# Kernel optimization log

Hardware: AMD Instinct MI355X
Metric: run time of the kernel (lower is better)

## Reference

```python
import jax, jax.numpy as jnp
import numpy as np

B, S, D, H = 2, 2048, 1024, 16
DK = D // H  # 64


def setup_inputs() -> dict:
    key = jax.random.key(0)
    ks = jax.random.split(key, 12)
    inp = {
        "query": jax.random.normal(ks[0], (B, S, D), jnp.float32),
        "key": jax.random.normal(ks[1], (B, S, D), jnp.float32),
        "value": jax.random.normal(ks[2], (B, S, D), jnp.float32),
        "mask": jnp.ones((B, 1, S, S), jnp.float32),  # 1.0 = attend
    }
    sc = 1.0 / np.sqrt(D)
    inp["wq"] = jax.random.normal(ks[3], (D, D), jnp.float32) * sc
    inp["bq"] = jax.random.normal(ks[4], (D,), jnp.float32) * 0.01
    inp["wk"] = jax.random.normal(ks[5], (D, D), jnp.float32) * sc
    inp["bk"] = jax.random.normal(ks[6], (D,), jnp.float32) * 0.01
    inp["wv"] = jax.random.normal(ks[7], (D, D), jnp.float32) * sc
    inp["bv"] = jax.random.normal(ks[8], (D,), jnp.float32) * 0.01
    inp["wo"] = jax.random.normal(ks[9], (D, D), jnp.float32) * sc
    inp["bo"] = jax.random.normal(ks[10], (D,), jnp.float32) * 0.01
    return inp


def _split_heads(x):
    # [B, S, D] -> [B, H, S, DK]
    b, s, _ = x.shape
    return x.reshape(b, s, H, DK).transpose(0, 2, 1, 3)


def reference(query, key, value, mask, wq, bq, wk, bk, wv, bv, wo, bo):
    # Linear projections (torch Linear: x @ W.T + b)
    q = _split_heads(query @ wq.T + bq)   # [B,H,Sq,DK]
    k = _split_heads(key @ wk.T + bk)     # [B,H,Sk,DK]
    v = _split_heads(value @ wv.T + bv)   # [B,H,Sk,DK]

    attn = jnp.einsum('bhqd,bhkd->bhqk', q, k) / jnp.sqrt(jnp.float32(DK))
    # mask: 1.0 attend, 0.0 masked -> add finfo.min at masked positions
    inv = (1.0 - mask) * jnp.finfo(attn.dtype).min
    attn = attn + inv
    attention_weights = jax.nn.softmax(attn, axis=-1)  # [B,H,Sq,Sk]
    # dropout=0.0 (eval mode): identity
    ctx = jnp.einsum('bhqk,bhkd->bhqd', attention_weights, v)  # [B,H,Sq,DK]
    concat = ctx.transpose(0, 2, 1, 3).reshape(ctx.shape[0], ctx.shape[2], D)
    output = concat @ wo.T + bo
    return (output, attention_weights)
```

## Files before the change

### kernel.cpp

```cpp
#include <hip/hip_runtime.h>
#include <cstdint>

typedef short bf16x8 __attribute__((ext_vector_type(8)));
typedef short bf16x4 __attribute__((ext_vector_type(4)));
typedef float f32x4 __attribute__((ext_vector_type(4)));

#define NEG_MAX 3.402823466e38f
#define C_EXP2 0.1803368801111244f

__device__ __forceinline__ unsigned short f2bf(float f) {
  uint32_t u = __builtin_bit_cast(uint32_t, f);
  u += 0x7FFFu + ((u >> 16) & 1u);
  return (unsigned short)(u >> 16);
}

__device__ __forceinline__ float bf2f(unsigned short s) {
  return __builtin_bit_cast(float, (uint32_t)s << 16);
}

__device__ __forceinline__ bf16x8 pack8(float4 x, float4 y) {
  bf16x8 r;
  r[0] = (short)f2bf(x.x); r[1] = (short)f2bf(x.y); r[2] = (short)f2bf(x.z); r[3] = (short)f2bf(x.w);
  r[4] = (short)f2bf(y.x); r[5] = (short)f2bf(y.y); r[6] = (short)f2bf(y.z); r[7] = (short)f2bf(y.w);
  return r;
}

__global__ __launch_bounds__(256) void cvt_w(const float* __restrict__ wq, const float* __restrict__ wk,
                                             const float* __restrict__ wv, const float* __restrict__ wo,
                                             unsigned short* __restrict__ out) {
  int i = blockIdx.x * 256 + threadIdx.x;
  const int sel = i >> 18;
  const int idx = i & 0x3FFFF;
  const float* src = (sel == 0) ? wq : (sel == 1) ? wk : (sel == 2) ? wv : wo;
  float4 v = reinterpret_cast<const float4*>(src)[idx];
  ushort4 o;
  o.x = f2bf(v.x); o.y = f2bf(v.y); o.z = f2bf(v.z); o.w = f2bf(v.w);
  reinterpret_cast<ushort4*>(out)[i] = o;
}

__global__ __launch_bounds__(256) void mask_scan(const float* __restrict__ mask,
                                                 int* __restrict__ flags) {
  const int blk = blockIdx.x;
  const int kt = blk & 31, qt = (blk >> 5) & 31, b = blk >> 10;
  const float* base = mask + ((size_t)b * 2048 + qt * 64) * 2048 + kt * 64;
  const int t = threadIdx.x;
  const int row = t >> 2, c0 = (t & 3) * 16;
  const float4* p = reinterpret_cast<const float4*>(base + (size_t)row * 2048 + c0);
  bool ones = true;
#pragma unroll
  for (int i = 0; i < 4; ++i) {
    float4 v = p[i];
    ones = ones && (v.x == 1.f) && (v.y == 1.f) && (v.z == 1.f) && (v.w == 1.f);
  }
  unsigned long long ball = __ballot(ones);
  __shared__ int sf[4];
  if ((t & 63) == 0) sf[t >> 6] = (ball == ~0ull) ? 1 : 0;
  __syncthreads();
  if (t == 0) flags[blk] = sf[0] & sf[1] & sf[2] & sf[3];
}

__global__ __launch_bounds__(256) void gemm_qkv(const float* __restrict__ Aq,
                                                const float* __restrict__ Ak,
                                                const float* __restrict__ Av,
                                                const unsigned short* __restrict__ W3,
                                                const float* __restrict__ bq,
                                                const float* __restrict__ bk,
                                                const float* __restrict__ bv,
                                                unsigned short* __restrict__ Qbf,
                                                unsigned short* __restrict__ Kbf,
                                                unsigned short* __restrict__ Vtb) {
  constexpr int KD = 1024;
  __shared__ __align__(16) unsigned short Al[128 * 32];
  __shared__ __align__(16) unsigned short Bl[128 * 32];
  const int tid = threadIdx.x;
  const int l = tid & 63;
  const int w = tid >> 6;
  const int lr = l & 15;
  const int lg = l >> 4;
  const int gm = blockIdx.y;
  const int gn = blockIdx.x;
  const int z = blockIdx.z;
  const int wr = w >> 1;
  const int wc = w & 1;

  const float* Af = (z == 0) ? Aq : (z == 1) ? Ak : Av;
  const float* bias = (z == 0) ? bq : (z == 1) ? bk : bv;
  const unsigned short* Bw = W3 + (size_t)z * 1048576;
  unsigned short* Cb = (z == 0) ? Qbf : (z == 1) ? Kbf : Vtb;

  f32x4 acc[4][4];
#pragma unroll
  for (int m = 0; m < 4; ++m)
#pragma unroll
    for (int n = 0; n < 4; ++n) acc[m][n] = (f32x4){0.f, 0.f, 0.f, 0.f};

  const int c0 = w * 2;
  const int srow = (l >> 2);
  const int scol = (l & 3) * 8;
  const unsigned short* gB = Bw + (size_t)(gn * 128) * KD;

  const int arow = tid >> 1;
  const int ahalf = tid & 1;
  const float* gA = Af + (size_t)(gm * 128 + arow) * KD + ahalf * 16;

  float4 ap[4];
  {
    const float4* p = reinterpret_cast<const float4*>(gA);
#pragma unroll
    for (int i = 0; i < 4; ++i) ap[i] = p[i];
  }

  for (int kt = 0; kt < 32; ++kt) {
    const int k0 = kt * 32;
    const unsigned short* b0 = gB + (size_t)(c0 * 16 + srow) * KD + k0 + scol;
    const unsigned short* b1 = b0 + (size_t)16 * KD;
    __builtin_amdgcn_global_load_lds((const __attribute__((address_space(1))) void*)b0,
                                     (__attribute__((address_space(3))) void*)&Bl[c0 * 512], 16, 0, 0);
    __builtin_amdgcn_global_load_lds((const __attribute__((address_space(1))) void*)b1,
                                     (__attribute__((address_space(3))) void*)&Bl[c0 * 512 + 512], 16, 0, 0);
    {
      bf16x8* dst = reinterpret_cast<bf16x8*>(&Al[arow * 32 + ahalf * 16]);
      dst[0] = pack8(ap[0], ap[1]);
      dst[1] = pack8(ap[2], ap[3]);
    }
    __syncthreads();
    if (kt + 1 < 32) {
      const float4* p = reinterpret_cast<const float4*>(gA + (kt + 1) * 32);
#pragma unroll
      for (int i = 0; i < 4; ++i) ap[i] = p[i];
    }
    bf16x8 af[4], bfr[4];
#pragma unroll
    for (int m = 0; m < 4; ++m)
      af[m] = *reinterpret_cast<const bf16x8*>(&Al[(wr * 64 + m * 16 + lr) * 32 + lg * 8]);
#pragma unroll
    for (int n = 0; n < 4; ++n)
      bfr[n] = *reinterpret_cast<const bf16x8*>(&Bl[(wc * 64 + n * 16 + lr) * 32 + lg * 8]);
#pragma unroll
    for (int m = 0; m < 4; ++m)
#pragma unroll
      for (int n = 0; n < 4; ++n)
        acc[m][n] = __builtin_amdgcn_mfma_f32_16x16x32_bf16(af[m], bfr[n], acc[m][n], 0, 0, 0);
    __syncthreads();
  }

#pragma unroll
  for (int m = 0; m < 4; ++m) {
#pragma unroll
    for (int n = 0; n < 4; ++n) {
      const int colg = gn * 128 + wc * 64 + n * 16 + lr;
      const float bv2 = bias[colg];
#pragma unroll
      for (int r = 0; r < 4; ++r) {
        const int rowg = gm * 128 + wr * 64 + m * 16 + lg * 4 + r;
        const float v = acc[m][n][r] + bv2;
        const int bb = rowg >> 11, ss = rowg & 2047;
        const int hh = colg >> 6, dk = colg & 63;
        if (z < 2)
          Cb[(((size_t)bb * 16 + hh) * 2048 + ss) * 64 + dk] = f2bf(v);
        else
          Cb[(((size_t)bb * 16 + hh) * 32 + (ss >> 6)) * 4096 + (size_t)dk * 64 + (ss & 63)] = f2bf(v);
      }
    }
  }
}

__global__ __launch_bounds__(256) void gemm_out(const unsigned short* __restrict__ A,
                                                const unsigned short* __restrict__ Bw,
                                                const float* __restrict__ bias,
                                                float* __restrict__ Cf) {
  constexpr int KD = 1024;
  __shared__ __align__(16) unsigned short Al[128 * 32];
  __shared__ __align__(16) unsigned short Bl[128 * 32];
  const int tid = threadIdx.x;
  const int l = tid & 63;
  const int w = tid >> 6;
  const int lr = l & 15;
  const int lg = l >> 4;
  const int gm = blockIdx.y;
  const int gn = blockIdx.x;
  const int wr = w >> 1;
  const int wc = w & 1;

  f32x4 acc[4][4];
#pragma unroll
  for (int m = 0; m < 4; ++m)
#pragma unroll
    for (int n = 0; n < 4; ++n) acc[m][n] = (f32x4){0.f, 0.f, 0.f, 0.f};

  const int c0 = w * 2;
  const int srow = (l >> 2);
  const int scol = (l & 3) * 8;
  const unsigned short* gA = A + (size_t)(gm * 128) * KD;
  const unsigned short* gB = Bw + (size_t)(gn * 128) * KD;

  for (int kt = 0; kt < 32; ++kt) {
    const int k0 = kt * 32;
    const unsigned short* a0 = gA + (size_t)(c0 * 16 + srow) * KD + k0 + scol;
    const unsigned short* a1 = a0 + (size_t)16 * KD;
    const unsigned short* b0 = gB + (size_t)(c0 * 16 + srow) * KD + k0 + scol;
    const unsigned short* b1 = b0 + (size_t)16 * KD;
    __builtin_amdgcn_global_load_lds((const __attribute__((address_space(1))) void*)a0,
                                     (__attribute__((address_space(3))) void*)&Al[c0 * 512], 16, 0, 0);
    __builtin_amdgcn_global_load_lds((const __attribute__((address_space(1))) void*)a1,
                                     (__attribute__((address_space(3))) void*)&Al[c0 * 512 + 512], 16, 0, 0);
    __builtin_amdgcn_global_load_lds((const __attribute__((address_space(1))) void*)b0,
                                     (__attribute__((address_space(3))) void*)&Bl[c0 * 512], 16, 0, 0);
    __builtin_amdgcn_global_load_lds((const __attribute__((address_space(1))) void*)b1,
                                     (__attribute__((address_space(3))) void*)&Bl[c0 * 512 + 512], 16, 0, 0);
    __syncthreads();
    bf16x8 af[4], bfr[4];
#pragma unroll
    for (int m = 0; m < 4; ++m)
      af[m] = *reinterpret_cast<const bf16x8*>(&Al[(wr * 64 + m * 16 + lr) * 32 + lg * 8]);
#pragma unroll
    for (int n = 0; n < 4; ++n)
      bfr[n] = *reinterpret_cast<const bf16x8*>(&Bl[(wc * 64 + n * 16 + lr) * 32 + lg * 8]);
#pragma unroll
    for (int m = 0; m < 4; ++m)
#pragma unroll
      for (int n = 0; n < 4; ++n)
        acc[m][n] = __builtin_amdgcn_mfma_f32_16x16x32_bf16(af[m], bfr[n], acc[m][n], 0, 0, 0);
    __syncthreads();
  }

#pragma unroll
  for (int m = 0; m < 4; ++m) {
#pragma unroll
    for (int n = 0; n < 4; ++n) {
      const int colg = gn * 128 + wc * 64 + n * 16 + lr;
      const float bv = bias[colg];
#pragma unroll
      for (int r = 0; r < 4; ++r) {
        const int rowg = gm * 128 + wr * 64 + m * 16 + lg * 4 + r;
        Cf[(size_t)rowg * 1024 + colg] = acc[m][n][r] + bv;
      }
    }
  }
}

__global__ __launch_bounds__(512, 4) void attn_fused(const unsigned short* __restrict__ Q,
                                                     const unsigned short* __restrict__ Kb,
                                                     const unsigned short* __restrict__ Vt,
                                                     const float* __restrict__ mask,
                                                     const int* __restrict__ flags,
                                                     float* __restrict__ wout,
                                                     unsigned short* __restrict__ ctx) {
  const int tid = threadIdx.x;
  const int l = tid & 63;
  const int w = tid >> 6;
  const int lr = l & 15;
  const int lg = l >> 4;

  const int d = blockIdx.x;
  const int bh = (d >> 7) * 8 + (d & 7);
  const int qp = (d >> 3) & 15;
  const int b = bh >> 4, h = bh & 15;
  const int q0 = qp * 128;

  __shared__ __align__(16) unsigned short KV[6][4096];
  __shared__ __align__(16) unsigned short Wl[8][16][64];

  const size_t qoff = ((size_t)bh * 2048 + (q0 + w * 16 + lr)) * 64 + lg * 8;
  const bf16x8 qf0 = *reinterpret_cast<const bf16x8*>(Q + qoff);
  const bf16x8 qf1 = *reinterpret_cast<const bf16x8*>(Q + qoff + 32);

  const int seg = tid;
  const int rs = seg >> 3, cx = (seg & 7) ^ (rs & 7);
  const unsigned short* kB = Kb + (size_t)bh * 131072;
  const unsigned short* vB = Vt + (size_t)bh * 131072;
  const size_t tS = (size_t)rs * 64 + cx * 8;
  const int ldsOff = w * 512;

  const int sA = (lg ^ (lr & 7)) << 3;
  const int sBo = ((4 + lg) ^ (lr & 7)) << 3;

  const int fbase = (b * 32 + qp * 2 + (w >> 2)) * 32;
  const uint32_t fmask = (uint32_t)__ballot(flags[fbase + (l & 31)] != 0);

  const float* mbase = mask + (size_t)b * 2048 * 2048;

  const int lc = l & 15;
  const int wsub = (lc & 1) * 4;
  const int wcch = lc >> 1;

#define STAGE(base_, kt_, slot_)                                                                       \
  do {                                                                                                 \
    __builtin_amdgcn_global_load_lds(                                                                  \
        (const __attribute__((address_space(1))) void*)((base_) + (size_t)(kt_) * 4096 + tS),          \
        (__attribute__((address_space(3))) void*)(&KV[slot_][0] + ldsOff), 16, 0, 0);                  \
  } while (0)

  float s0[4] = {0.f, 0.f, 0.f, 0.f};

  STAGE(kB, 0, 0);
  STAGE(kB, 1, 1);
  STAGE(kB, 2, 2);
  STAGE(kB, 3, 3);
  for (int it = 0; it < 16; ++it) {
    if (it < 15) {
      asm volatile("s_waitcnt vmcnt(2)" ::: "memory");
    } else {
      asm volatile("s_waitcnt vmcnt(0)" ::: "memory");
    }
    __builtin_amdgcn_s_barrier();
    __builtin_amdgcn_sched_barrier(0);
    const int kt0 = it * 2;
#pragma unroll
    for (int half = 0; half < 2; ++half) {
      const int kt = kt0 + half;
      const unsigned short* Ks = &KV[kt % 6][0];
      bf16x8 kf0[4], kf1[4];
#pragma unroll
      for (int n = 0; n < 4; ++n) {
        const int rb = (n * 16 + lr) * 64;
        kf0[n] = *reinterpret_cast<const bf16x8*>(&Ks[rb + sA]);
        kf1[n] = *reinterpret_cast<const bf16x8*>(&Ks[rb + sBo]);
      }
      if (kt + 4 < 32) STAGE(kB, kt + 4, (kt + 4) % 6);
      f32x4 acc[4];
#pragma unroll
      for (int n = 0; n < 4; ++n) {
        acc[n] = (f32x4){0.f, 0.f, 0.f, 0.f};
        acc[n] = __builtin_amdgcn_mfma_f32_16x16x32_bf16(qf0, kf0[n], acc[n], 0, 0, 0);
        acc[n] = __builtin_amdgcn_mfma_f32_16x16x32_bf16(qf1, kf1[n], acc[n], 0, 0, 0);
      }
      if ((fmask >> kt) & 1) {
#pragma unroll
        for (int r = 0; r < 4; ++r)
          s0[r] += exp2f(acc[0][r] * C_EXP2) + exp2f(acc[1][r] * C_EXP2) +
                   exp2f(acc[2][r] * C_EXP2) + exp2f(acc[3][r] * C_EXP2);
      } else {
#pragma unroll
        for (int r = 0; r < 4; ++r) {
          const int qrow = q0 + w * 16 + lg * 4 + r;
          const float* mp = mbase + (size_t)qrow * 2048 + kt * 64;
          float ps = 0.f;
#pragma unroll
          for (int n = 0; n < 4; ++n) {
            const float mv = mp[n * 16 + lr];
            ps += __expf(acc[n][r] * 0.125f + (1.0f - mv) * (-NEG_MAX));
          }
          s0[r] += ps;
        }
      }
    }
  }

  float inv_s[4];
#pragma unroll
  for (int r = 0; r < 4; ++r) {
#pragma unroll
    for (int dd = 1; dd < 16; dd <<= 1) s0[r] += __shfl_xor(s0[r], dd);
    inv_s[r] = 1.0f / s0[r];
  }

  f32x4 cacc[4];
#pragma unroll
  for (int n = 0; n < 4; ++n) cacc[n] = (f32x4){0.f, 0.f, 0.f, 0.f};

  STAGE(kB, 0, 0);
  STAGE(vB, 0, 2);
  for (int kt = 0; kt < 32; ++kt) {
    const int cur = kt & 1;
    if (kt == 0) {
      asm volatile("s_waitcnt vmcnt(0)" ::: "memory");
    } else {
      asm volatile("s_waitcnt vmcnt(4)" ::: "memory");
    }
    __builtin_amdgcn_s_barrier();
    __builtin_amdgcn_sched_barrier(0);
    const unsigned short* Ks = &KV[cur][0];
    const unsigned short* Vs = &KV[2 + cur][0];
    bf16x8 kf0[4], kf1[4];
#pragma unroll
    for (int n = 0; n < 4; ++n) {
      const int rb = (n * 16 + lr) * 64;
      kf0[n] = *reinterpret_cast<const bf16x8*>(&Ks[rb + sA]);
      kf1[n] = *reinterpret_cast<const bf16x8*>(&Ks[rb + sBo]);
    }
    if (kt + 1 < 32) {
      STAGE(kB, kt + 1, cur ^ 1);
      STAGE(vB, kt + 1, 2 + (cur ^ 1));
    }
    f32x4 acc[4];
#pragma unroll
    for (int n = 0; n < 4; ++n) {
      acc[n] = (f32x4){0.f, 0.f, 0.f, 0.f};
      acc[n] = __builtin_amdgcn_mfma_f32_16x16x32_bf16(qf0, kf0[n], acc[n], 0, 0, 0);
      acc[n] = __builtin_amdgcn_mfma_f32_16x16x32_bf16(qf1, kf1[n], acc[n], 0, 0, 0);
    }
    const int fl = (fmask >> kt) & 1;
#pragma unroll
    for (int r = 0; r < 4; ++r) {
      const int row2 = lg * 4 + r;
      const int rx = (row2 & 7) << 3;
      if (fl) {
#pragma unroll
        for (int n = 0; n < 4; ++n) {
          const float wgt = exp2f(acc[n][r] * C_EXP2) * inv_s[r];
          Wl[w][row2][(n * 16 + lr) ^ rx] = f2bf(wgt);
        }
      } else {
        const int qrow = q0 + w * 16 + row2;
        const float* mp = mbase + (size_t)qrow * 2048 + kt * 64;
#pragma unroll
        for (int n = 0; n < 4; ++n) {
          const float mv = mp[n * 16 + lr];
          const float wgt = __expf(acc[n][r] * 0.125f + (1.0f - mv) * (-NEG_MAX)) * inv_s[r];
          Wl[w][row2][(n * 16 + lr) ^ rx] = f2bf(wgt);
        }
      }
    }
    bf16x8 vf0[4], vf1[4];
#pragma unroll
    for (int n = 0; n < 4; ++n) {
      const int rb = (n * 16 + lr) * 64;
      vf0[n] = *reinterpret_cast<const bf16x8*>(&Vs[rb + sA]);
      vf1[n] = *reinterpret_cast<const bf16x8*>(&Vs[rb + sBo]);
    }
    asm volatile("s_waitcnt lgkmcnt(0)" ::: "memory");
    __builtin_amdgcn_sched_barrier(0);
    {
#pragma unroll
      for (int i = 0; i < 4; ++i) {
        const int row = i * 4 + (l >> 4);
        const int addr = ((wcch ^ (row & 7)) << 3) + wsub;
        const bf16x4 wb = *reinterpret_cast<const bf16x4*>(&Wl[w][row][addr]);
        f32x4 fo;
        fo[0] = bf2f((unsigned short)wb[0]);
        fo[1] = bf2f((unsigned short)wb[1]);
        fo[2] = bf2f((unsigned short)wb[2]);
        fo[3] = bf2f((unsigned short)wb[3]);
        f32x4* wpv = reinterpret_cast<f32x4*>(
            wout + ((size_t)bh * 2048 + q0 + w * 16 + row) * 2048 + kt * 64 + lc * 4);
        __builtin_nontemporal_store(fo, wpv);
      }
    }
    const bf16x8 a0 = *reinterpret_cast<const bf16x8*>(&Wl[w][lr][(lg ^ (lr & 7)) * 8]);
    const bf16x8 a1 = *reinterpret_cast<const bf16x8*>(&Wl[w][lr][((4 | lg) ^ (lr & 7)) * 8]);
#pragma unroll
    for (int n = 0; n < 4; ++n) {
      cacc[n] = __builtin_amdgcn_mfma_f32_16x16x32_bf16(a0, vf0[n], cacc[n], 0, 0, 0);
      cacc[n] = __builtin_amdgcn_mfma_f32_16x16x32_bf16(a1, vf1[n], cacc[n], 0, 0, 0);
    }
  }

#pragma unroll
  for (int n = 0; n < 4; ++n) {
#pragma unroll
    for (int r = 0; r < 4; ++r) {
      const int ss = q0 + w * 16 + lg * 4 + r;
      const int col = h * 64 + n * 16 + lr;
      ctx[((size_t)b * 2048 + ss) * 1024 + col] = f2bf(cacc[n][r]);
    }
  }
#undef STAGE
}

extern "C" void kernel_launch(void* const* d_in, const int* in_sizes, int n_in,
                              void* d_out, int out_size, void* d_ws, size_t ws_size,
                              hipStream_t stream) {
  const float* query = (const float*)d_in[0];
  const float* key   = (const float*)d_in[1];
  const float* value = (const float*)d_in[2];
  const float* mask  = (const float*)d_in[3];
  const float* wq = (const float*)d_in[4];
  const float* bq = (const float*)d_in[5];
  const float* wk = (const float*)d_in[6];
  const float* bk = (const float*)d_in[7];
  const float* wv = (const float*)d_in[8];
  const float* bv = (const float*)d_in[9];
  const float* wo = (const float*)d_in[10];
  const float* bo = (const float*)d_in[11];

  unsigned short* Qbf = (unsigned short*)d_ws;
  unsigned short* Kbf = Qbf + 4194304;
  unsigned short* Vtb = Kbf + 4194304;
  unsigned short* ctx = Vtb + 4194304;
  unsigned short* wbf4 = ctx + 4194304;
  int* flags = (int*)(wbf4 + 4194304);

  float* outp = (float*)d_out;
  float* wout = outp + 4194304;

  mask_scan<<<2048, 256, 0, stream>>>(mask, flags);
  cvt_w<<<4096, 256, 0, stream>>>(wq, wk, wv, wo, wbf4);

  dim3 gq(8, 32, 3);
  gemm_qkv<<<gq, 256, 0, stream>>>(query, key, value, wbf4, bq, bk, bv, Qbf, Kbf, Vtb);

  attn_fused<<<512, 512, 0, stream>>>(Qbf, Kbf, Vtb, mask, flags, wout, ctx);

  dim3 gg(8, 32);
  gemm_out<<<gg, 256, 0, stream>>>(ctx, wbf4 + 3145728, bo, outp);
}
```

Measured before the change: 262.6 us.

## Split fused attention into separate denominator and PV kernels with key-split partial sums

The softmax denominator pass moves out of the fused attention kernel into its own kernel. That kernel uses 2048 smaller blocks, each covering 64 query rows and half of the keys, and writes partial row sums to workspace. The PV kernel reads and combines the two partials, and its shared-memory K/V buffer shrinks from 6 to 4 slots, allowing higher occupancy. The goal is more parallelism and less latency in the first pass, at the cost of an extra launch, a small global round-trip for the sums, and reloading Q.

```diff
diff --git a/kernel.cpp b/kernel.cpp
--- a/kernel.cpp
+++ b/kernel.cpp
@@ -239,13 +239,11 @@
   }
 }
 
-__global__ __launch_bounds__(512, 4) void attn_fused(const unsigned short* __restrict__ Q,
+__global__ __launch_bounds__(256, 6) void attn_denom(const unsigned short* __restrict__ Q,
                                                      const unsigned short* __restrict__ Kb,
-                                                     const unsigned short* __restrict__ Vt,
                                                      const float* __restrict__ mask,
                                                      const int* __restrict__ flags,
-                                                     float* __restrict__ wout,
-                                                     unsigned short* __restrict__ ctx) {
+                                                     float* __restrict__ spart) {
   const int tid = threadIdx.x;
   const int l = tid & 63;
   const int w = tid >> 6;
@@ -253,12 +251,129 @@
   const int lg = l >> 4;
 
   const int d = blockIdx.x;
+  const int bh = (d >> 9) * 8 + (d & 7);
+  const int qt = (d >> 4) & 31;
+  const int ks = (d >> 3) & 1;
+  const int b = bh >> 4;
+  const int q0 = qt * 64;
+  const int ktbase = ks * 16;
+
+  __shared__ __align__(16) unsigned short Kl[3][4096];
+
+  const size_t qoff = ((size_t)bh * 2048 + (q0 + w * 16 + lr)) * 64 + lg * 8;
+  const bf16x8 qf0 = *reinterpret_cast<const bf16x8*>(Q + qoff);
+  const bf16x8 qf1 = *reinterpret_cast<const bf16x8*>(Q + qoff + 32);
+
+  const int seg0 = w * 128 + l;
+  const int seg1 = seg0 + 64;
+  const int r0s = seg0 >> 3, c0x = (seg0 & 7) ^ (r0s & 7);
+  const int r1s = seg1 >> 3, c1x = (seg1 & 7) ^ (r1s & 7);
+  const unsigned short* kB = Kb + (size_t)bh * 131072;
+  const size_t tS0 = (size_t)r0s * 64 + c0x * 8;
+  const size_t tS1 = (size_t)r1s * 64 + c1x * 8;
+  const int ldsOff0 = w * 1024;
+  const int ldsOff1 = w * 1024 + 512;
+
+  const int sA = (lg ^ (lr & 7)) << 3;
+  const int sBo = ((4 + lg) ^ (lr & 7)) << 3;
+
+  const int fbase = (b * 32 + qt) * 32 + ktbase;
+  const uint32_t fmask = (uint32_t)__ballot(flags[fbase + (l & 15)] != 0);
+
+  const float* mbase = mask + (size_t)b * 2048 * 2048;
+
+#define STAGEK(i_, slot_)                                                                              \
+  do {                                                                                                 \
+    const unsigned short* s_ = kB + (size_t)(ktbase + (i_)) * 4096;                                    \
+    __builtin_amdgcn_global_load_lds((const __attribute__((address_space(1))) void*)(s_ + tS0),        \
+                                     (__attribute__((address_space(3))) void*)(&Kl[slot_][0] + ldsOff0), 16, 0, 0); \
+    __builtin_amdgcn_global_load_lds((const __attribute__((address_space(1))) void*)(s_ + tS1),        \
+                                     (__attribute__((address_space(3))) void*)(&Kl[slot_][0] + ldsOff1), 16, 0, 0); \
+  } while (0)
+
+  float s0[4] = {0.f, 0.f, 0.f, 0.f};
+
+  STAGEK(0, 0);
+  STAGEK(1, 1);
+  for (int it = 0; it < 16; ++it) {
+    if (it < 15) {
+      asm volatile("s_waitcnt vmcnt(2)" ::: "memory");
+    } else {
+      asm volatile("s_waitcnt vmcnt(0)" ::: "memory");
+    }
+    __builtin_amdgcn_s_barrier();
+    __builtin_amdgcn_sched_barrier(0);
+    const unsigned short* Ks = &Kl[it % 3][0];
+    bf16x8 kf0[4], kf1[4];
+#pragma unroll
+    for (int n = 0; n < 4; ++n) {
+      const int rb = (n * 16 + lr) * 64;
+      kf0[n] = *reinterpret_cast<const bf16x8*>(&Ks[rb + sA]);
+      kf1[n] = *reinterpret_cast<const bf16x8*>(&Ks[rb + sBo]);
+    }
+    if (it + 2 < 16) STAGEK(it + 2, (it + 2) % 3);
+    f32x4 acc[4];
+#pragma unroll
+    for (int n = 0; n < 4; ++n) {
+      acc[n] = (f32x4){0.f, 0.f, 0.f, 0.f};
+      acc[n] = __builtin_amdgcn_mfma_f32_16x16x32_bf16(qf0, kf0[n], acc[n], 0, 0, 0);
+      acc[n] = __builtin_amdgcn_mfma_f32_16x16x32_bf16(qf1, kf1[n], acc[n], 0, 0, 0);
+    }
+    if ((fmask >> it) & 1) {
+#pragma unroll
+      for (int r = 0; r < 4; ++r)
+        s0[r] += exp2f(acc[0][r] * C_EXP2) + exp2f(acc[1][r] * C_EXP2) +
+                 exp2f(acc[2][r] * C_EXP2) + exp2f(acc[3][r] * C_EXP2);
+    } else {
+#pragma unroll
+      for (int r = 0; r < 4; ++r) {
+        const int qrow = q0 + w * 16 + lg * 4 + r;
+        const float* mp = mbase + (size_t)qrow * 2048 + (ktbase + it) * 64;
+        float ps = 0.f;
+#pragma unroll
+        for (int n = 0; n < 4; ++n) {
+          const float mv = mp[n * 16 + lr];
+          ps += __expf(acc[n][r] * 0.125f + (1.0f - mv) * (-NEG_MAX));
+        }
+        s0[r] += ps;
+      }
+    }
+  }
+
+#pragma unroll
+  for (int r = 0; r < 4; ++r) {
+#pragma unroll
+    for (int dd = 1; dd < 16; dd <<= 1) s0[r] += __shfl_xor(s0[r], dd);
+  }
+  if (lr == 0) {
+#pragma unroll
+    for (int r = 0; r < 4; ++r)
+      spart[(size_t)ks * 65536 + (size_t)bh * 2048 + q0 + w * 16 + lg * 4 + r] = s0[r];
+  }
+#undef STAGEK
+}
+
+__global__ __launch_bounds__(512, 6) void attn_pv(const unsigned short* __restrict__ Q,
+                                                  const unsigned short* __restrict__ Kb,
+                                                  const unsigned short* __restrict__ Vt,
+                                                  const float* __restrict__ mask,
+                                                  const int* __restrict__ flags,
+                                                  const float* __restrict__ spart,
+                                                  float* __restrict__ wout,
+                                                  unsigned short* __restrict__ ctx) {
+  const int tid = threadIdx.x;
+  const int l = tid & 63;
+  const int w = tid >> 6;
+  const int lr = l & 15;
+  const int lg = l >> 4;
+
+  const int d = blockIdx.x;
   const int bh = (d >> 7) * 8 + (d & 7);
   const int qp = (d >> 3) & 15;
   const int b = bh >> 4, h = bh & 15;
   const int q0 = qp * 128;
 
-  __shared__ __align__(16) unsigned short KV[6][4096];
+  __shared__ __align__(16) unsigned short KV[4][4096];
   __shared__ __align__(16) unsigned short Wl[8][16][64];
 
   const size_t qoff = ((size_t)bh * 2048 + (q0 + w * 16 + lr)) * 64 + lg * 8;
@@ -280,6 +395,13 @@
 
   const float* mbase = mask + (size_t)b * 2048 * 2048;
 
+  float inv_s[4];
+#pragma unroll
+  for (int r = 0; r < 4; ++r) {
+    const int row = q0 + w * 16 + lg * 4 + r;
+    inv_s[r] = 1.0f / (spart[(size_t)bh * 2048 + row] + spart[65536 + (size_t)bh * 2048 + row]);
+  }
+
   const int lc = l & 15;
   const int wsub = (lc & 1) * 4;
   const int wcch = lc >> 1;
@@ -290,70 +412,6 @@
         (const __attribute__((address_space(1))) void*)((base_) + (size_t)(kt_) * 4096 + tS),          \
         (__attribute__((address_space(3))) void*)(&KV[slot_][0] + ldsOff), 16, 0, 0);                  \
   } while (0)
-
-  float s0[4] = {0.f, 0.f, 0.f, 0.f};
-
-  STAGE(kB, 0, 0);
-  STAGE(kB, 1, 1);
-  STAGE(kB, 2, 2);
-  STAGE(kB, 3, 3);
-  for (int it = 0; it < 16; ++it) {
-    if (it < 15) {
-      asm volatile("s_waitcnt vmcnt(2)" ::: "memory");
-    } else {
-      asm volatile("s_waitcnt vmcnt(0)" ::: "memory");
-    }
-    __builtin_amdgcn_s_barrier();
-    __builtin_amdgcn_sched_barrier(0);
-    const int kt0 = it * 2;
-#pragma unroll
-    for (int half = 0; half < 2; ++half) {
-      const int kt = kt0 + half;
-      const unsigned short* Ks = &KV[kt % 6][0];
-      bf16x8 kf0[4], kf1[4];
-#pragma unroll
-      for (int n = 0; n < 4; ++n) {
-        const int rb = (n * 16 + lr) * 64;
-        kf0[n] = *reinterpret_cast<const bf16x8*>(&Ks[rb + sA]);
-        kf1[n] = *reinterpret_cast<const bf16x8*>(&Ks[rb + sBo]);
-      }
-      if (kt + 4 < 32) STAGE(kB, kt + 4, (kt + 4) % 6);
-      f32x4 acc[4];
-#pragma unroll
-      for (int n = 0; n < 4; ++n) {
-        acc[n] = (f32x4){0.f, 0.f, 0.f, 0.f};
-        acc[n] = __builtin_amdgcn_mfma_f32_16x16x32_bf16(qf0, kf0[n], acc[n], 0, 0, 0);
-        acc[n] = __builtin_amdgcn_mfma_f32_16x16x32_bf16(qf1, kf1[n], acc[n], 0, 0, 0);
-      }
-      if ((fmask >> kt) & 1) {
-#pragma unroll
-        for (int r = 0; r < 4; ++r)
-          s0[r] += exp2f(acc[0][r] * C_EXP2) + exp2f(acc[1][r] * C_EXP2) +
-                   exp2f(acc[2][r] * C_EXP2) + exp2f(acc[3][r] * C_EXP2);
-      } else {
-#pragma unroll
-        for (int r = 0; r < 4; ++r) {
-          const int qrow = q0 + w * 16 + lg * 4 + r;
-          const float* mp = mbase + (size_t)qrow * 2048 + kt * 64;
-          float ps = 0.f;
-#pragma unroll
-          for (int n = 0; n < 4; ++n) {
-            const float mv = mp[n * 16 + lr];
-            ps += __expf(acc[n][r] * 0.125f + (1.0f - mv) * (-NEG_MAX));
-          }
-          s0[r] += ps;
-        }
-      }
-    }
-  }
-
-  float inv_s[4];
-#pragma unroll
-  for (int r = 0; r < 4; ++r) {
-#pragma unroll
-    for (int dd = 1; dd < 16; dd <<= 1) s0[r] += __shfl_xor(s0[r], dd);
-    inv_s[r] = 1.0f / s0[r];
-  }
 
   f32x4 cacc[4];
 #pragma unroll
@@ -480,6 +538,7 @@
   unsigned short* ctx = Vtb + 4194304;
   unsigned short* wbf4 = ctx + 4194304;
   int* flags = (int*)(wbf4 + 4194304);
+  float* spart = (float*)(flags + 2048);
 
   float* outp = (float*)d_out;
   float* wout = outp + 4194304;
@@ -490,7 +549,8 @@
   dim3 gq(8, 32, 3);
   gemm_qkv<<<gq, 256, 0, stream>>>(query, key, value, wbf4, bq, bk, bv, Qbf, Kbf, Vtb);
 
-  attn_fused<<<512, 512, 0, stream>>>(Qbf, Kbf, Vtb, mask, flags, wout, ctx);
+  attn_denom<<<2048, 256, 0, stream>>>(Qbf, Kbf, mask, flags, spart);
+  attn_pv<<<512, 512, 0, stream>>>(Qbf, Kbf, Vtb, mask, flags, spart, wout, ctx);
 
   dim3 gg(8, 32);
   gemm_out<<<gg, 256, 0, stream>>>(ctx, wbf4 + 3145728, bo, outp);
```

Result: slower. 419.7 us (+59.8%).
